# Performance work log

Measured on AMD Instinct MI355X. Metric: run time of the kernel, lower is better.

## Reference

```python
import jax, jax.numpy as jnp
import numpy as np

EMB = 1024
HEAD = 64  # emb_size // head_nb = 1024 // 16

def setup_inputs() -> dict:
    key = jax.random.key(0)
    kx, kq, kk, kv = jax.random.split(key, 4)
    x = jax.random.normal(kx, (8, 2048, EMB), dtype=jnp.float32)
    # torch nn.Linear(EMB, HEAD) weight has shape [HEAD, EMB]; y = x @ W.T
    s = 1.0 / np.sqrt(EMB)
    Wq = jax.random.uniform(kq, (HEAD, EMB), jnp.float32, -s, s)
    Wk = jax.random.uniform(kk, (HEAD, EMB), jnp.float32, -s, s)
    Wv = jax.random.uniform(kv, (HEAD, EMB), jnp.float32, -s, s)
    return {"x": x, "Wq": Wq, "Wk": Wk, "Wv": Wv}

def reference(x, Wq, Wk, Wv):
    B, T, C = x.shape
    q = jnp.einsum('btc,hc->bth', x, Wq)  # [B,T,H]
    k = jnp.einsum('btc,hc->bth', x, Wk)
    v = jnp.einsum('btc,hc->bth', x, Wv)
    scale = 1.0 / jnp.sqrt(jnp.float32(q.shape[-1]))
    wei = jnp.einsum('bth,bsh->bts', q, k) * scale  # [B,T,T]
    causal = jnp.tril(jnp.ones((T, T), dtype=bool))
    wei = jnp.where(causal, wei, -jnp.inf)
    wei = jax.nn.softmax(wei, axis=-1)
    # dropout is identity in eval mode
    out = jnp.einsum('bts,bsh->bth', wei, v)  # [B,T,H]
    return out
```

## Files before the change

### kernel.cpp

```cpp
#include <hip/hip_runtime.h>
#include <math.h>

#define SEQ  2048
#define NROW 16384
#define HEAD 64
#define EMB  1024

typedef __attribute__((ext_vector_type(8))) short short8;
typedef __attribute__((ext_vector_type(4))) float f32x4;

static __device__ __forceinline__ unsigned short f2bf(float f) {
    unsigned u = __builtin_bit_cast(unsigned, f);
    u += 0x7fffu + ((u >> 16) & 1u);
    return (unsigned short)(u >> 16);
}
static __device__ __forceinline__ float bf2f(unsigned short u) {
    unsigned v = (unsigned)u << 16;
    return __builtin_bit_cast(float, v);
}
static __device__ __forceinline__ ushort4 cvt4(float4 f) {
    ushort4 u;
    u.x = f2bf(f.x); u.y = f2bf(f.y); u.z = f2bf(f.z); u.w = f2bf(f.w);
    return u;
}

static __device__ __forceinline__ void gload_lds16(const void* g, void* l) {
    __builtin_amdgcn_global_load_lds(
        (const __attribute__((address_space(1))) unsigned int*)g,
        (__attribute__((address_space(3))) unsigned int*)l, 16, 0, 0);
}

__global__ __launch_bounds__(256) void wcvt_kernel(
    const float* __restrict__ Wq, const float* __restrict__ Wk,
    const float* __restrict__ Wv, unsigned short* __restrict__ Wb)
{
    const int idx = (blockIdx.x * 256 + threadIdx.x) * 4;
    const int h = idx >> 10;
    const float* src;
    if (h < 64)       src = Wq + idx;
    else if (h < 128) src = Wk + (idx - 65536);
    else              src = Wv + (idx - 131072);
    *(ushort4*)(Wb + idx) = cvt4(*(const float4*)src);
}

__global__ __launch_bounds__(512, 2) void qkv_mfma_kernel(
    const float* __restrict__ x, const unsigned short* __restrict__ Wb,
    unsigned short* __restrict__ qN, unsigned short* __restrict__ kN,
    unsigned short* __restrict__ vT)
{
    __shared__ unsigned short As[2][64][72];
    __shared__ unsigned short Bs[2][192 * 64];

    const int tid  = threadIdx.x;
    const int w    = tid >> 6;
    const int lane = tid & 63;
    const int col  = lane & 15;
    const int quad = lane >> 4;
    const int row0 = blockIdx.x * 64;
    const int wm   = w >> 2;
    const int wn   = w & 3;
    const int pq   = (quad ^ (col & 7)) * 8;

    const int ar_r = tid >> 4, ar_c = tid & 15;
    const float* xg = x + (size_t)(row0 + ar_r) * EMB + ar_c * 4;

    const int sr = lane >> 3, cc = (lane & 7) ^ sr;
    const unsigned short* bg = Wb;

    {
        float4 fa[2];
#pragma unroll
        for (int j = 0; j < 2; ++j) fa[j] = *(const float4*)(xg + (size_t)(32 * j) * EMB);
#pragma unroll
        for (int j = 0; j < 2; ++j) *(ushort4*)&As[0][ar_r + 32 * j][ar_c * 4] = cvt4(fa[j]);
#pragma unroll
        for (int j = 0; j < 3; ++j) {
            const int c = w * 3 + j;
            gload_lds16(bg + (size_t)(c * 8 + sr) * EMB + cc * 8,
                        &Bs[0][c * 8 * 64]);
        }
    }
    __syncthreads();

    f32x4 acc[2][3];
#pragma unroll
    for (int mf = 0; mf < 2; ++mf)
#pragma unroll
        for (int t = 0; t < 3; ++t) acc[mf][t] = (f32x4){0.f, 0.f, 0.f, 0.f};

    float4 fa[2];
#pragma unroll 2
    for (int kt = 0; kt < 16; ++kt) {
        const int cur = kt & 1;
        if (kt + 1 < 16) {
            const int k0 = (kt + 1) * 64;
#pragma unroll
            for (int j = 0; j < 3; ++j) {
                const int c = w * 3 + j;
                gload_lds16(bg + (size_t)(c * 8 + sr) * EMB + k0 + cc * 8,
                            &Bs[cur ^ 1][c * 8 * 64]);
            }
#pragma unroll
            for (int j = 0; j < 2; ++j)
                fa[j] = *(const float4*)(xg + (size_t)(32 * j) * EMB + k0);
        }
#pragma unroll
        for (int ks = 0; ks < 2; ++ks) {
            short8 af0 = *(const short8*)&As[cur][wm * 32 + col][ks * 32 + quad * 8];
            short8 af1 = *(const short8*)&As[cur][wm * 32 + 16 + col][ks * 32 + quad * 8];
            const int po = pq ^ (ks * 32);
#pragma unroll
            for (int t = 0; t < 3; ++t) {
                short8 bf = *(const short8*)
                    &Bs[cur][(wn * 48 + t * 16 + col) * 64 + po];
                acc[0][t] = __builtin_amdgcn_mfma_f32_16x16x32_bf16(af0, bf, acc[0][t], 0, 0, 0);
                acc[1][t] = __builtin_amdgcn_mfma_f32_16x16x32_bf16(af1, bf, acc[1][t], 0, 0, 0);
            }
        }
        if (kt + 1 < 16) {
#pragma unroll
            for (int j = 0; j < 2; ++j)
                *(ushort4*)&As[cur ^ 1][ar_r + 32 * j][ar_c * 4] = cvt4(fa[j]);
        }
        __syncthreads();
    }

#pragma unroll
    for (int mf = 0; mf < 2; ++mf) {
        const int ro = row0 + wm * 32 + mf * 16 + quad * 4;
#pragma unroll
        for (int t = 0; t < 3; ++t) {
            const int hb = wn * 48 + 16 * t;
            const int h  = hb + col;
            if (hb < 64) {
#pragma unroll
                for (int r = 0; r < 4; ++r)
                    qN[(size_t)(ro + r) * HEAD + h] = f2bf(acc[mf][t][r] * 0.125f);
            } else if (hb < 128) {
#pragma unroll
                for (int r = 0; r < 4; ++r)
                    kN[(size_t)(ro + r) * HEAD + (h - 64)] = f2bf(acc[mf][t][r]);
            } else {
                ushort4 uv;
                uv.x = f2bf(acc[mf][t][0]); uv.y = f2bf(acc[mf][t][1]);
                uv.z = f2bf(acc[mf][t][2]); uv.w = f2bf(acc[mf][t][3]);
                *(ushort4*)(vT + (size_t)(h - 128) * NROW + ro) = uv;
            }
        }
    }
}

__global__ __launch_bounds__(256, 3) void attn_kernel(
    const unsigned short* __restrict__ qN,
    const unsigned short* __restrict__ kN,
    const unsigned short* __restrict__ vT,
    unsigned short* __restrict__ op,
    float2* __restrict__ ml)
{
    __shared__ unsigned short Ks[2][64 * 64];
    __shared__ unsigned short Vs[2][64 * 64];
    __shared__ unsigned short Pl[4][32][72];

    const int qt   = 15 - (int)blockIdx.x;
    const int b    = blockIdx.y;
    const int p    = blockIdx.z;
    const int tid  = threadIdx.x;
    const int wv   = tid >> 6;
    const int lane = tid & 63;
    const int col  = lane & 15;
    const int quad = lane >> 4;

    const int q0   = qt * 128 + wv * 16;
    const int q0g  = b * SEQ + q0;
    const int Cb   = 2 * qt + 2;
    const int kt0  = (Cb * p) >> 2;
    const int kt1  = (Cb * (p + 1)) >> 2;
    const int ktp  = min(kt0, Cb - 1);

    const int sr = lane >> 3, cc = (lane & 7) ^ sr;
    const int pq = (quad ^ (col & 7)) * 8;
    const unsigned short* kgb = kN + (size_t)(b * SEQ) * HEAD;
    const int bcol = b * SEQ;

    const short8* qp0 = (const short8*)qN + (size_t)(q0g + col) * 8;
    const short8* qp1 = (const short8*)qN + (size_t)(q0g + 64 + col) * 8;
    short8 aq00 = qp0[quad], aq01 = qp0[quad + 4];
    short8 aq10 = qp1[quad], aq11 = qp1[quad + 4];

    f32x4 o[2][4];
    float l_i[2][4];
#pragma unroll
    for (int mi = 0; mi < 2; ++mi)
#pragma unroll
        for (int t = 0; t < 4; ++t) {
            o[mi][t] = (f32x4){0.f, 0.f, 0.f, 0.f};
            l_i[mi][t] = 0.f;
        }

#pragma unroll
    for (int j = 0; j < 2; ++j) {
        const int r = (wv * 2 + j) * 8 + sr;
        gload_lds16(kgb + (size_t)(ktp * 64 + r) * HEAD + cc * 8,
                    &Ks[0][(wv * 2 + j) * 8 * 64]);
        gload_lds16(vT + (size_t)r * NROW + bcol + ktp * 64 + cc * 8,
                    &Vs[0][(wv * 2 + j) * 8 * 64]);
    }
    __syncthreads();

    for (int kt = kt0; kt < kt1; ++kt) {
        const int cur = (kt - kt0) & 1;
        const int s0  = kt * 64;
        const bool dz = (kt >= Cb - 2);
        const bool m0 = (kt < Cb - 1);

        if (kt + 1 < kt1) {
#pragma unroll
            for (int j = 0; j < 2; ++j) {
                const int r = (wv * 2 + j) * 8 + sr;
                gload_lds16(kgb + (size_t)((kt + 1) * 64 + r) * HEAD + cc * 8,
                            &Ks[cur ^ 1][(wv * 2 + j) * 8 * 64]);
                gload_lds16(vT + (size_t)r * NROW + bcol + (kt + 1) * 64 + cc * 8,
                            &Vs[cur ^ 1][(wv * 2 + j) * 8 * 64]);
            }
        }

        f32x4 sv[2][4];
#pragma unroll
        for (int t = 0; t < 4; ++t) {
            sv[0][t] = (f32x4){0.f, 0.f, 0.f, 0.f};
            sv[1][t] = (f32x4){0.f, 0.f, 0.f, 0.f};
        }
#pragma unroll
        for (int t = 0; t < 4; ++t) {
            const int rb = (16 * t + col) * 64;
            short8 kf0 = *(const short8*)&Ks[cur][rb + pq];
            short8 kf1 = *(const short8*)&Ks[cur][rb + (pq ^ 32)];
            sv[1][t] = __builtin_amdgcn_mfma_f32_16x16x32_bf16(aq10, kf0, sv[1][t], 0, 0, 0);
            sv[1][t] = __builtin_amdgcn_mfma_f32_16x16x32_bf16(aq11, kf1, sv[1][t], 0, 0, 0);
            if (m0) {
                sv[0][t] = __builtin_amdgcn_mfma_f32_16x16x32_bf16(aq00, kf0, sv[0][t], 0, 0, 0);
                sv[0][t] = __builtin_amdgcn_mfma_f32_16x16x32_bf16(aq01, kf1, sv[0][t], 0, 0, 0);
            }
        }

#pragma unroll
        for (int mi = 0; mi < 2; ++mi) {
            if (mi == 0 && !m0) continue;
#pragma unroll
            for (int r = 0; r < 4; ++r) {
                const int grow = q0 + mi * 64 + quad * 4 + r;
                float ls = 0.f;
#pragma unroll
                for (int t = 0; t < 4; ++t) {
                    float e = __expf(sv[mi][t][r]);
                    if (dz && (s0 + 16 * t + col > grow)) e = 0.0f;
                    Pl[wv][mi * 16 + quad * 4 + r][16 * t + col] = f2bf(e);
                    ls += e;
                }
                l_i[mi][r] += ls;
            }
        }

        short8 pf00, pf01;
        if (m0) {
            pf00 = *(const short8*)&Pl[wv][col][quad * 8];
            pf01 = *(const short8*)&Pl[wv][col][quad * 8 + 32];
        }
        short8 pf10 = *(const short8*)&Pl[wv][16 + col][quad * 8];
        short8 pf11 = *(const short8*)&Pl[wv][16 + col][quad * 8 + 32];

#pragma unroll
        for (int tn = 0; tn < 4; ++tn) {
            const int rb = (16 * tn + col) * 64;
            short8 vf0 = *(const short8*)&Vs[cur][rb + pq];
            short8 vf1 = *(const short8*)&Vs[cur][rb + (pq ^ 32)];
            o[1][tn] = __builtin_amdgcn_mfma_f32_16x16x32_bf16(pf10, vf0, o[1][tn], 0, 0, 0);
            o[1][tn] = __builtin_amdgcn_mfma_f32_16x16x32_bf16(pf11, vf1, o[1][tn], 0, 0, 0);
            if (m0) {
                o[0][tn] = __builtin_amdgcn_mfma_f32_16x16x32_bf16(pf00, vf0, o[0][tn], 0, 0, 0);
                o[0][tn] = __builtin_amdgcn_mfma_f32_16x16x32_bf16(pf01, vf1, o[0][tn], 0, 0, 0);
            }
        }

        __syncthreads();
    }

#pragma unroll
    for (int mi = 0; mi < 2; ++mi) {
#pragma unroll
        for (int r = 0; r < 4; ++r) {
            float l = l_i[mi][r];
            l += __shfl_xor(l, 1, 16);
            l += __shfl_xor(l, 2, 16);
            l += __shfl_xor(l, 4, 16);
            l += __shfl_xor(l, 8, 16);
            l_i[mi][r] = l;
        }
        const int ro = q0g + mi * 64 + quad * 4;
#pragma unroll
        for (int tn = 0; tn < 4; ++tn)
#pragma unroll
            for (int r = 0; r < 4; ++r)
                op[((size_t)p * NROW + ro + r) * HEAD + 16 * tn + col] =
                    f2bf(o[mi][tn][r]);
        if (col == 0) {
#pragma unroll
            for (int r = 0; r < 4; ++r)
                ml[p * NROW + ro + r] = make_float2(0.0f, l_i[mi][r]);
        }
    }
}

__global__ __launch_bounds__(256) void merge_kernel(
    const unsigned short* __restrict__ op, const float2* __restrict__ ml,
    float* __restrict__ out)
{
    const int idx = blockIdx.x * 256 + threadIdx.x;
    const int row = idx >> 4;
    const int hc  = (idx & 15) * 4;

    float denom = 0.0f;
#pragma unroll
    for (int p = 0; p < 4; ++p) denom += ml[p * NROW + row].y;
    const float inv = 1.0f / denom;

    float4 r = make_float4(0.f, 0.f, 0.f, 0.f);
#pragma unroll
    for (int p = 0; p < 4; ++p) {
        ushort4 u = *(const ushort4*)(op + ((size_t)p * NROW + row) * HEAD + hc);
        r.x += bf2f(u.x);
        r.y += bf2f(u.y);
        r.z += bf2f(u.z);
        r.w += bf2f(u.w);
    }
    r.x *= inv; r.y *= inv; r.z *= inv; r.w *= inv;
    *(float4*)(out + (size_t)row * HEAD + hc) = r;
}

extern "C" void kernel_launch(void* const* d_in, const int* in_sizes, int n_in,
                              void* d_out, int out_size, void* d_ws, size_t ws_size,
                              hipStream_t stream)
{
    const float* x  = (const float*)d_in[0];
    const float* Wq = (const float*)d_in[1];
    const float* Wk = (const float*)d_in[2];
    const float* Wv = (const float*)d_in[3];

    char* w = (char*)d_ws;
    unsigned short* qN = (unsigned short*)w;
    unsigned short* kN = (unsigned short*)(w + (2u << 20));
    unsigned short* vT = (unsigned short*)(w + (4u << 20));
    unsigned short* Wb = (unsigned short*)(w + (6u << 20));
    unsigned short* op = (unsigned short*)(w + (6u << 20) + 393216);
    float2*         ml = (float2*)(w + (14u << 20) + 393216);
    float* out = (float*)d_out;

    wcvt_kernel<<<192, 256, 0, stream>>>(Wq, Wk, Wv, Wb);
    qkv_mfma_kernel<<<256, 512, 0, stream>>>(x, Wb, qN, kN, vT);
    attn_kernel<<<dim3(16, 8, 4), 256, 0, stream>>>(qN, kN, vT, op, ml);
    merge_kernel<<<1024, 256, 0, stream>>>(op, ml, out);
}
```

Baseline: 137.4 us.

## Stage x tiles via async global-to-LDS loads with triple buffering

The QKV projection kernel now loads raw fp32 x tiles straight into LDS with global_load_lds (XOR-swizzled) rather than through registers, and converts to bf16 only when reading MFMA fragments. The pipeline grows from double to triple buffering with explicit vmcnt waits and raw barriers, keeping two stages in flight. The aim is to remove register staging and conversion stalls from the load path and hide global memory latency better. In exchange it doubles LDS per A tile (fp32) plus a third buffer, which may lower occupancy under launch_bounds(512,2), and it repeats the conversion work for each wave that reads the same tile.

```diff
diff --git a/kernel.cpp b/kernel.cpp
--- a/kernel.cpp
+++ b/kernel.cpp
@@ -17,6 +17,12 @@
 static __device__ __forceinline__ float bf2f(unsigned short u) {
     unsigned v = (unsigned)u << 16;
     return __builtin_bit_cast(float, v);
+}
+static __device__ __forceinline__ short8 cvt8(float4 a, float4 b) {
+    short8 r;
+    r[0] = f2bf(a.x); r[1] = f2bf(a.y); r[2] = f2bf(a.z); r[3] = f2bf(a.w);
+    r[4] = f2bf(b.x); r[5] = f2bf(b.y); r[6] = f2bf(b.z); r[7] = f2bf(b.w);
+    return r;
 }
 static __device__ __forceinline__ ushort4 cvt4(float4 f) {
     ushort4 u;
@@ -48,8 +54,8 @@
     unsigned short* __restrict__ qN, unsigned short* __restrict__ kN,
     unsigned short* __restrict__ vT)
 {
-    __shared__ unsigned short As[2][64][72];
-    __shared__ unsigned short Bs[2][192 * 64];
+    __shared__ float          Asf[3][64 * 64];
+    __shared__ unsigned short Bs[3][192 * 64];
 
     const int tid  = threadIdx.x;
     const int w    = tid >> 6;
@@ -61,26 +67,30 @@
     const int wn   = w & 3;
     const int pq   = (quad ^ (col & 7)) * 8;
 
-    const int ar_r = tid >> 4, ar_c = tid & 15;
-    const float* xg = x + (size_t)(row0 + ar_r) * EMB + ar_c * 4;
-
+    const int r_loc = lane >> 4, cslot = lane & 15;
     const int sr = lane >> 3, cc = (lane & 7) ^ sr;
-    const unsigned short* bg = Wb;
-
-    {
-        float4 fa[2];
-#pragma unroll
-        for (int j = 0; j < 2; ++j) fa[j] = *(const float4*)(xg + (size_t)(32 * j) * EMB);
-#pragma unroll
-        for (int j = 0; j < 2; ++j) *(ushort4*)&As[0][ar_r + 32 * j][ar_c * 4] = cvt4(fa[j]);
-#pragma unroll
-        for (int j = 0; j < 3; ++j) {
-            const int c = w * 3 + j;
-            gload_lds16(bg + (size_t)(c * 8 + sr) * EMB + cc * 8,
-                        &Bs[0][c * 8 * 64]);
-        }
-    }
-    __syncthreads();
+
+#define STAGE(buf, k0) do {                                                   \
+    _Pragma("unroll")                                                         \
+    for (int j_ = 0; j_ < 2; ++j_) {                                          \
+        const int rr_ = w * 8 + j_ * 4 + r_loc;                               \
+        const int cs_ = cslot ^ (j_ * 4 + r_loc);                             \
+        gload_lds16(x + (size_t)(row0 + rr_) * EMB + (k0) + cs_ * 4,          \
+                    (char*)&Asf[buf][0] + (w * 8 + j_ * 4) * 256);            \
+    }                                                                         \
+    _Pragma("unroll")                                                         \
+    for (int j_ = 0; j_ < 3; ++j_) {                                          \
+        const int c_ = w * 3 + j_;                                            \
+        gload_lds16(Wb + (size_t)(c_ * 8 + sr) * EMB + (k0) + cc * 8,         \
+                    &Bs[buf][c_ * 8 * 64]);                                   \
+    }                                                                         \
+} while (0)
+
+    STAGE(0, 0);
+    STAGE(1, 64);
+    asm volatile("s_waitcnt vmcnt(5)" ::: "memory");
+    __builtin_amdgcn_sched_barrier(0);
+    __builtin_amdgcn_s_barrier();
 
     f32x4 acc[2][3];
 #pragma unroll
@@ -88,26 +98,24 @@
 #pragma unroll
         for (int t = 0; t < 3; ++t) acc[mf][t] = (f32x4){0.f, 0.f, 0.f, 0.f};
 
-    float4 fa[2];
-#pragma unroll 2
+    const int x7   = col & 7;
+    const int rbA0 = (wm * 32 + col) * 16;
+    const int rbA1 = (wm * 32 + 16 + col) * 16;
+
+#pragma unroll
     for (int kt = 0; kt < 16; ++kt) {
-        const int cur = kt & 1;
-        if (kt + 1 < 16) {
-            const int k0 = (kt + 1) * 64;
-#pragma unroll
-            for (int j = 0; j < 3; ++j) {
-                const int c = w * 3 + j;
-                gload_lds16(bg + (size_t)(c * 8 + sr) * EMB + k0 + cc * 8,
-                            &Bs[cur ^ 1][c * 8 * 64]);
-            }
-#pragma unroll
-            for (int j = 0; j < 2; ++j)
-                fa[j] = *(const float4*)(xg + (size_t)(32 * j) * EMB + k0);
-        }
+        const int cur = kt % 3;
+        if (kt + 2 < 16) STAGE((kt + 2) % 3, (kt + 2) * 64);
+        const float4* Ap = (const float4*)&Asf[cur][0];
 #pragma unroll
         for (int ks = 0; ks < 2; ++ks) {
-            short8 af0 = *(const short8*)&As[cur][wm * 32 + col][ks * 32 + quad * 8];
-            short8 af1 = *(const short8*)&As[cur][wm * 32 + 16 + col][ks * 32 + quad * 8];
+            const int c0 = ks * 8 + quad * 2;
+            float4 a00 = Ap[rbA0 + (c0 ^ x7)];
+            float4 a01 = Ap[rbA0 + ((c0 + 1) ^ x7)];
+            float4 a10 = Ap[rbA1 + (c0 ^ x7)];
+            float4 a11 = Ap[rbA1 + ((c0 + 1) ^ x7)];
+            short8 af0 = cvt8(a00, a01);
+            short8 af1 = cvt8(a10, a11);
             const int po = pq ^ (ks * 32);
 #pragma unroll
             for (int t = 0; t < 3; ++t) {
@@ -117,13 +125,14 @@
                 acc[1][t] = __builtin_amdgcn_mfma_f32_16x16x32_bf16(af1, bf, acc[1][t], 0, 0, 0);
             }
         }
-        if (kt + 1 < 16) {
-#pragma unroll
-            for (int j = 0; j < 2; ++j)
-                *(ushort4*)&As[cur ^ 1][ar_r + 32 * j][ar_c * 4] = cvt4(fa[j]);
-        }
-        __syncthreads();
-    }
+        if (kt < 15) {
+            if (kt <= 13) asm volatile("s_waitcnt vmcnt(5) lgkmcnt(0)" ::: "memory");
+            else          asm volatile("s_waitcnt vmcnt(0) lgkmcnt(0)" ::: "memory");
+            __builtin_amdgcn_sched_barrier(0);
+            __builtin_amdgcn_s_barrier();
+        }
+    }
+#undef STAGE
 
 #pragma unroll
     for (int mf = 0; mf < 2; ++mf) {
```

Result: no change. 138.6 us (+0.9%).
